# Performance work log

Hardware: AMD Instinct MI355X
Metric: run time of the kernel (lower is better)

The kernel has to match this reference:

```python
import jax, jax.numpy as jnp
import numpy as np

WK = 5        # fine_window_size
STRIDE = 4    # hardcoded in forward
PAD = WK // 2


def _gather_windows(feat, b, idx):
    # feat: [N, C, H, W]; b, idx: [M]. Replicates F.unfold(k=5, s=4, p=2)
    # followed by permute/reshape(n, l, W^2, c) and advanced indexing,
    # but only materializes the M selected windows (fused unfold+gather).
    N, C, H, W = feat.shape
    out_w = (W + 2 * PAD - WK) // STRIDE + 1
    fp = jnp.pad(feat, ((0, 0), (0, 0), (PAD, PAD), (PAD, PAD)))
    gy = idx // out_w
    gx = idx % out_w
    rows = gy[:, None] * STRIDE + jnp.arange(WK)   # [M, WK]
    cols = gx[:, None] * STRIDE + jnp.arange(WK)   # [M, WK]
    # advanced indices at axes 0,2,3 with slice at axis 1 -> [M, WK, WK, C]
    patch = fp[b[:, None, None], :, rows[:, :, None], cols[:, None, :]]
    # F.unfold flattens channel-major (C, kh, kw); the torch code then
    # reshapes that C*WK*WK axis as (WK*WK, C) -- an index-mixing reshape
    # we must replicate exactly.
    M = b.shape[0]
    patch = patch.transpose(0, 3, 1, 2).reshape(M, C * WK * WK)
    return patch.reshape(M, WK * WK, C)


def setup_inputs() -> dict:
    key = jax.random.key(0)
    k0, k1, kb, ki, kj = jax.random.split(key, 5)
    N, C, H, W = 4, 128, 240, 320
    L = (H // STRIDE) * (W // STRIDE)  # 4800 coarse positions
    M = 6000
    return {
        "feat_f0": jax.random.normal(k0, (N, C, H, W), dtype=jnp.float32),
        "feat_f1": jax.random.normal(k1, (N, C, H, W), dtype=jnp.float32),
        "hw0_f": jnp.array([H, W], dtype=jnp.int64),
        "hw0_c": jnp.array([H // STRIDE, W // STRIDE], dtype=jnp.int64),
        "b_ids": jax.random.randint(kb, (M,), 0, N, dtype=jnp.int64),
        "i_ids": jax.random.randint(ki, (M,), 0, L, dtype=jnp.int64),
        "j_ids": jax.random.randint(kj, (M,), 0, L, dtype=jnp.int64),
    }


def reference(feat_f0, feat_f1, hw0_f, hw0_c, b_ids, i_ids, j_ids):
    feat0 = _gather_windows(feat_f0, b_ids, i_ids)  # [M, W^2, C]
    feat1 = _gather_windows(feat_f1, b_ids, j_ids)  # [M, W^2, C]
    return feat0, feat1
```

## Files before the change

### kernel.cpp

```cpp
#include <hip/hip_runtime.h>


#define MPTS 6000
#define NPTS (2 * MPTS)
#define NCH  128
#define FH   240
#define FW   320
#define OUTW 80
#define OUTH 60
#define NKEY (2 * 4 * OUTH)
#define PTFLOATS (NCH * 25)

#define WS_HIST   0
#define WS_CURSOR 512
#define WS_BASE   1024
#define WS_ORDER  2048
#define WS_INTS   (WS_ORDER + NPTS)

typedef float f2 __attribute__((ext_vector_type(2)));

__device__ __forceinline__ int point_key(int map, int b, int gy) {
    return (map * 4 + b) * OUTH + gy;
}


__global__ void k_zero(int* __restrict__ ws) {
    const int t = threadIdx.x;
    if (t < WS_BASE) ws[t] = 0;
}

__global__ void k_hist(const int* __restrict__ b_ids,
                       const int* __restrict__ i_ids,
                       const int* __restrict__ j_ids,
                       int* __restrict__ ws) {
    const int t = blockIdx.x * blockDim.x + threadIdx.x;
    if (t >= NPTS) return;
    const int map = t >= MPTS;
    const int m   = map ? t - MPTS : t;
    const int idx = map ? j_ids[m] : i_ids[m];
    const int gy  = idx / OUTW;
    atomicAdd(&ws[WS_HIST + point_key(map, b_ids[m], gy)], 1);
}

__global__ void k_scan(int* __restrict__ ws) {
    __shared__ int h[NKEY];
    const int t = threadIdx.x;
    for (int i = t; i < NKEY; i += blockDim.x) h[i] = ws[WS_HIST + i];
    __syncthreads();
    if (t == 0) {
        int acc = 0;
        for (int i = 0; i < NKEY; i++) { int v = h[i]; h[i] = acc; acc += v; }
    }
    __syncthreads();
    for (int i = t; i < NKEY; i += blockDim.x) ws[WS_BASE + i] = h[i];
    if (t == 0) ws[WS_BASE + NKEY] = NPTS;
}

__global__ void k_scatter(const int* __restrict__ b_ids,
                          const int* __restrict__ i_ids,
                          const int* __restrict__ j_ids,
                          int* __restrict__ ws) {
    const int t = blockIdx.x * blockDim.x + threadIdx.x;
    if (t >= NPTS) return;
    const int map = t >= MPTS;
    const int m   = map ? t - MPTS : t;
    const int idx = map ? j_ids[m] : i_ids[m];
    const int gy  = idx / OUTW;
    const int key = point_key(map, b_ids[m], gy);
    const int pos = atomicAdd(&ws[WS_CURSOR + key], 1);
    ws[WS_ORDER + ws[WS_BASE + key] + pos] = t;
}


__global__ __launch_bounds__(320) void fine_gather_kernel(
    const float* __restrict__ f0, const float* __restrict__ f1,
    const int* __restrict__ b_ids, const int* __restrict__ i_ids,
    const int* __restrict__ j_ids, const int* __restrict__ order,
    float* __restrict__ out)
{
    __shared__ __align__(16) float lds[PTFLOATS];

    int ent;
    if (order) {
        const int pos = (blockIdx.x & 7) * (NPTS / 8) + (blockIdx.x >> 3);
        ent = order[pos];
    } else {
        ent = blockIdx.x;
    }

    const int map = ent >= MPTS;
    const int m   = map ? ent - MPTS : ent;
    const float* __restrict__ feat = map ? f1 : f0;
    const int idx = map ? j_ids[m] : i_ids[m];
    const int b   = b_ids[m];

    const int gy = idx / OUTW;
    const int gx = idx - gy * OUTW;
    const int row0 = gy * 4 - 2;
    const int col0 = gx * 4 - 2;

    const int t = threadIdx.x;

#pragma unroll
    for (int it = 0; it < 2; it++) {
        const int s = t + it * 320;
        const int c = s / 5;
        const int r = s - c * 5;
        const int row = row0 + r;
        const bool vrow = (row >= 0) & (row < FH);
        const float* src = feat + (((long)(b * NCH + c) * FH + row) * FW + col0);

        float v[5];
        if (vrow && (col0 >= 0)) {
            const float4* p = (const float4*)(src - 2);
            const float4 q0 = p[0];
            const float4 q1 = p[1];
            v[0] = q0.z; v[1] = q0.w; v[2] = q1.x; v[3] = q1.y; v[4] = q1.z;
        } else {
#pragma unroll
            for (int k = 0; k < 5; k++) {
                const int cc = col0 + k;
                v[k] = (vrow && cc >= 0) ? src[k] : 0.0f;
            }
        }
        const int base = s * 5;
#pragma unroll
        for (int k = 0; k < 5; k++) lds[base + k] = v[k];
    }

    __syncthreads();

    float4* __restrict__ dst = (float4*)(out + (long)ent * PTFLOATS);
    const float4* sl = (const float4*)lds;
    for (int i = t; i < PTFLOATS / 4; i += 320)
        dst[i] = sl[i];
}


extern "C" void kernel_launch(void* const* d_in, const int* in_sizes, int n_in,
                              void* d_out, int out_size, void* d_ws, size_t ws_size,
                              hipStream_t stream) {
    const float* f0   = (const float*)d_in[0];
    const float* f1   = (const float*)d_in[1];
    const int* b_ids  = (const int*)d_in[4];
    const int* i_ids  = (const int*)d_in[5];
    const int* j_ids  = (const int*)d_in[6];
    float* out        = (float*)d_out;

    int* ws = (int*)d_ws;
    const bool have_ws = (ws != nullptr) && (ws_size >= (size_t)WS_INTS * sizeof(int));

    const int* order = nullptr;
    if (have_ws) {
        k_zero<<<1, 1024, 0, stream>>>(ws);
        k_hist<<<(NPTS + 255) / 256, 256, 0, stream>>>(b_ids, i_ids, j_ids, ws);
        k_scan<<<1, 512, 0, stream>>>(ws);
        k_scatter<<<(NPTS + 255) / 256, 256, 0, stream>>>(b_ids, i_ids, j_ids, ws);
        order = ws + WS_ORDER;
    }

    fine_gather_kernel<<<NPTS, 320, 0, stream>>>(f0, f1, b_ids, i_ids, j_ids, order, out);
}
```

Measured before the change: 405.6 us.

## Process four points per block with register double-buffering and drop LDS staging

Each block now handles four consecutive points from the sorted order instead of one. The next point's window is loaded into registers while the current point is stored, which overlaps load latency with stores. The shared-memory staging and barrier are removed: each thread writes its 5 contiguous floats directly using an unaligned float4 store plus a scalar store. This gives fewer, longer blocks and drops the LDS round trip, at the cost of less coalesced, unaligned global stores and higher register use under a launch_bounds occupancy hint.

After: 426.3 us. 1.05x slower.

```diff
diff --git a/kernel.cpp b/kernel.cpp
--- a/kernel.cpp
+++ b/kernel.cpp
@@ -11,13 +11,18 @@
 #define NKEY (2 * 4 * OUTH)
 #define PTFLOATS (NCH * 25)
 
+#define PTS_PER_BLK 4
+#define NBLK (NPTS / PTS_PER_BLK)
+#define PER_XCD (NPTS / 8)
+
 #define WS_HIST   0
 #define WS_CURSOR 512
 #define WS_BASE   1024
 #define WS_ORDER  2048
 #define WS_INTS   (WS_ORDER + NPTS)
 
-typedef float f2 __attribute__((ext_vector_type(2)));
+typedef float f4_t __attribute__((ext_vector_type(4)));
+typedef f4_t uf4 __attribute__((aligned(4)));
 
 __device__ __forceinline__ int point_key(int map, int b, int gy) {
     return (map * 4 + b) * OUTH + gy;
@@ -72,22 +77,13 @@
 }
 
 
-__global__ __launch_bounds__(320) void fine_gather_kernel(
+__device__ __forceinline__ void load_point(
     const float* __restrict__ f0, const float* __restrict__ f1,
     const int* __restrict__ b_ids, const int* __restrict__ i_ids,
     const int* __restrict__ j_ids, const int* __restrict__ order,
-    float* __restrict__ out)
+    int pos, int t, long& obase, float v[2][5])
 {
-    __shared__ __align__(16) float lds[PTFLOATS];
-
-    int ent;
-    if (order) {
-        const int pos = (blockIdx.x & 7) * (NPTS / 8) + (blockIdx.x >> 3);
-        ent = order[pos];
-    } else {
-        ent = blockIdx.x;
-    }
-
+    const int ent = order ? order[pos] : pos;
     const int map = ent >= MPTS;
     const int m   = map ? ent - MPTS : ent;
     const float* __restrict__ feat = map ? f1 : f0;
@@ -98,8 +94,7 @@
     const int gx = idx - gy * OUTW;
     const int row0 = gy * 4 - 2;
     const int col0 = gx * 4 - 2;
-
-    const int t = threadIdx.x;
+    obase = (long)ent * PTFLOATS;
 
 #pragma unroll
     for (int it = 0; it < 2; it++) {
@@ -110,30 +105,65 @@
         const bool vrow = (row >= 0) & (row < FH);
         const float* src = feat + (((long)(b * NCH + c) * FH + row) * FW + col0);
 
-        float v[5];
         if (vrow && (col0 >= 0)) {
             const float4* p = (const float4*)(src - 2);
             const float4 q0 = p[0];
             const float4 q1 = p[1];
-            v[0] = q0.z; v[1] = q0.w; v[2] = q1.x; v[3] = q1.y; v[4] = q1.z;
+            v[it][0] = q0.z; v[it][1] = q0.w;
+            v[it][2] = q1.x; v[it][3] = q1.y; v[it][4] = q1.z;
         } else {
 #pragma unroll
             for (int k = 0; k < 5; k++) {
                 const int cc = col0 + k;
-                v[k] = (vrow && cc >= 0) ? src[k] : 0.0f;
+                v[it][k] = (vrow && cc >= 0) ? src[k] : 0.0f;
             }
         }
-        const int base = s * 5;
+    }
+}
+
+__device__ __forceinline__ void store_point(
+    float* __restrict__ out, long obase, int t, const float v[2][5])
+{
 #pragma unroll
-        for (int k = 0; k < 5; k++) lds[base + k] = v[k];
+    for (int it = 0; it < 2; it++) {
+        const int s = t + it * 320;
+        float* dst = out + obase + (long)s * 5;
+        uf4 q;
+        q.x = v[it][0]; q.y = v[it][1]; q.z = v[it][2]; q.w = v[it][3];
+        *(uf4*)dst = q;
+        dst[4] = v[it][4];
     }
+}
 
-    __syncthreads();
+__global__ __launch_bounds__(320, 7) void fine_gather_kernel(
+    const float* __restrict__ f0, const float* __restrict__ f1,
+    const int* __restrict__ b_ids, const int* __restrict__ i_ids,
+    const int* __restrict__ j_ids, const int* __restrict__ order,
+    float* __restrict__ out)
+{
+    const int blk = blockIdx.x;
+    const int base_pos = (blk & 7) * PER_XCD + (blk >> 3) * PTS_PER_BLK;
+    const int t = threadIdx.x;
 
-    float4* __restrict__ dst = (float4*)(out + (long)ent * PTFLOATS);
-    const float4* sl = (const float4*)lds;
-    for (int i = t; i < PTFLOATS / 4; i += 320)
-        dst[i] = sl[i];
+    long obase_a; float va[2][5];
+    load_point(f0, f1, b_ids, i_ids, j_ids, order, base_pos, t, obase_a, va);
+
+#pragma unroll
+    for (int p = 0; p < PTS_PER_BLK; p++) {
+        long obase_b; float vb[2][5];
+        if (p + 1 < PTS_PER_BLK) {
+            load_point(f0, f1, b_ids, i_ids, j_ids, order,
+                       base_pos + p + 1, t, obase_b, vb);
+        }
+        store_point(out, obase_a, t, va);
+        if (p + 1 < PTS_PER_BLK) {
+            obase_a = obase_b;
+#pragma unroll
+            for (int it = 0; it < 2; it++)
+#pragma unroll
+                for (int k = 0; k < 5; k++) va[it][k] = vb[it][k];
+        }
+    }
 }
 
 
@@ -159,5 +189,5 @@
         order = ws + WS_ORDER;
     }
 
-    fine_gather_kernel<<<NPTS, 320, 0, stream>>>(f0, f1, b_ids, i_ids, j_ids, order, out);
+    fine_gather_kernel<<<NBLK, 320, 0, stream>>>(f0, f1, b_ids, i_ids, j_ids, order, out);
 }
```
